# Performance work log

Measured on AMD Instinct MI355X. Metric: run time of the kernel, lower is better.

The kernel has to match this reference:

```python
import jax, jax.numpy as jnp
import numpy as np

N_NODES = 50000
N_GRAPHS = 50
MAX_NODES = 1000  # equal-size graphs
C_IN = 128
C_OUT = 128
N_EDGES = 800000
N_LAYERS = 3
BN_EPS = 1e-5


def setup_inputs() -> dict:
    key = jax.random.key(0)
    ks = jax.random.split(key, 20)
    x = jax.random.normal(ks[0], (N_NODES, C_IN), dtype=jnp.float32)
    edge_index = jax.random.randint(ks[1], (2, N_EDGES), 0, N_NODES, dtype=jnp.int64)
    batch = jnp.repeat(jnp.arange(N_GRAPHS, dtype=jnp.int64), MAX_NODES)
    s_in = 1.0 / np.sqrt(C_IN)
    s_out = 1.0 / np.sqrt(C_OUT)
    fh_W = jax.random.normal(ks[2], (C_IN, C_OUT), dtype=jnp.float32) * s_in
    fh_b = jnp.zeros((C_OUT,), dtype=jnp.float32)
    W1 = jax.random.normal(ks[3], (N_LAYERS, C_OUT, C_OUT), dtype=jnp.float32) * s_out
    b1 = jnp.zeros((N_LAYERS, C_OUT), dtype=jnp.float32)
    g1 = jnp.ones((N_LAYERS, C_OUT), dtype=jnp.float32)
    be1 = jnp.zeros((N_LAYERS, C_OUT), dtype=jnp.float32)
    W2 = jax.random.normal(ks[4], (N_LAYERS, C_OUT, C_OUT), dtype=jnp.float32) * s_out
    b2 = jnp.zeros((N_LAYERS, C_OUT), dtype=jnp.float32)
    g2 = jnp.ones((N_LAYERS, C_OUT), dtype=jnp.float32)
    be2 = jnp.zeros((N_LAYERS, C_OUT), dtype=jnp.float32)
    return {"x": x, "edge_index": edge_index, "batch": batch,
            "fh_W": fh_W, "fh_b": fh_b,
            "W1": W1, "b1": b1, "g1": g1, "be1": be1,
            "W2": W2, "b2": b2, "g2": g2, "be2": be2}


def _bn(h, gamma, beta):
    # training-mode BatchNorm1d over the node dim (biased variance, like torch)
    mu = jnp.mean(h, axis=0)
    var = jnp.var(h, axis=0)
    return (h - mu) * jax.lax.rsqrt(var + BN_EPS) * gamma + beta


def _mlp(h, W1, b1, g1, be1, W2, b2, g2, be2):
    h = jax.nn.relu(_bn(h @ W1 + b1, g1, be1))
    h = jax.nn.relu(_bn(h @ W2 + b2, g2, be2))
    return h


def _to_dense_batch(h, batch):
    # counts per graph -> exclusive starts -> intra-graph position
    ones = jnp.ones((h.shape[0],), dtype=jnp.int32)
    counts = jax.ops.segment_sum(ones, batch, num_segments=N_GRAPHS)
    starts = jnp.cumsum(counts) - counts
    pos = jnp.arange(h.shape[0], dtype=jnp.int32) - starts[batch]
    dense = jnp.zeros((N_GRAPHS, MAX_NODES, h.shape[1]), dtype=h.dtype)
    return dense.at[batch, pos].set(h)


def reference(x, edge_index, batch, fh_W, fh_b, W1, b1, g1, be1, W2, b2, g2, be2):
    src, dst = edge_index[0], edge_index[1]
    h = x @ fh_W + fh_b  # first_head Linear
    outs = [_to_dense_batch(h, batch)]
    for l in range(N_LAYERS):
        # GINConv: mlp((1+eps)*x + sum_{j->i} x_j), eps=0
        agg = jax.ops.segment_sum(h[src], dst, num_segments=N_NODES)
        h = _mlp(h + agg, W1[l], b1[l], g1[l], be1[l], W2[l], b2[l], g2[l], be2[l])
        outs.append(_to_dense_batch(h, batch))
    return jnp.stack(outs)  # [N_LAYERS+1, B, MAX_NODES, C]
```

## Files before the change

### kernel.cpp

```cpp
#include <hip/hip_runtime.h>

#define NN 50000
#define NE 800000
#define CC 128
#define SLAB (NN * CC)
#define BN_EPS 1e-5f

typedef __attribute__((ext_vector_type(8))) short bf16x8;
typedef __attribute__((ext_vector_type(4))) float f32x4;
typedef unsigned short ushort_t;

__device__ inline ushort_t f2bf(float v) {
  unsigned u = __builtin_bit_cast(unsigned, v);
  unsigned r = u + 0x7FFFu + ((u >> 16) & 1u);
  return (ushort_t)(r >> 16);
}

__global__ void zero_int_kernel(int* __restrict__ p, int n) {
  int i = blockIdx.x * blockDim.x + threadIdx.x;
  if (i < n) p[i] = 0;
}

__global__ void count_kernel(const int* __restrict__ dst, int* __restrict__ counts) {
  int e = blockIdx.x * blockDim.x + threadIdx.x;
  if (e < NE) atomicAdd(&counts[dst[e]], 1);
}

__global__ void scan1_kernel(const int* __restrict__ counts, int* __restrict__ excl,
                             int* __restrict__ blocksum) {
  __shared__ int s[256];
  int t = threadIdx.x;
  int i = blockIdx.x * 256 + t;
  int v = (i < NN) ? counts[i] : 0;
  s[t] = v;
  for (int off = 1; off < 256; off <<= 1) {
    __syncthreads();
    int add = (t >= off) ? s[t - off] : 0;
    __syncthreads();
    s[t] += add;
  }
  __syncthreads();
  if (i < NN) excl[i] = s[t] - v;
  if (t == 255) blocksum[blockIdx.x] = s[255];
}

__global__ void scan2_kernel(int* __restrict__ blocksum, int nb) {
  __shared__ int s[256];
  int t = threadIdx.x;
  int v = (t < nb) ? blocksum[t] : 0;
  s[t] = v;
  for (int off = 1; off < 256; off <<= 1) {
    __syncthreads();
    int add = (t >= off) ? s[t - off] : 0;
    __syncthreads();
    s[t] += add;
  }
  __syncthreads();
  if (t < nb) blocksum[t] = s[t] - v;
}

__global__ void scan3_kernel(int* __restrict__ excl, const int* __restrict__ blocksum) {
  int i = blockIdx.x * 256 + threadIdx.x;
  if (i < NN) excl[i] += blocksum[blockIdx.x];
}

__global__ void fill_kernel(const int* __restrict__ src, const int* __restrict__ dst,
                            const int* __restrict__ starts, int* __restrict__ fill,
                            int* __restrict__ bucket) {
  int e = blockIdx.x * blockDim.x + threadIdx.x;
  if (e < NE) {
    int d = dst[e];
    int pos = atomicAdd(&fill[d], 1);
    bucket[starts[d] + pos] = src[e];
  }
}

__global__ void prep_w_kernel(const float* __restrict__ fh_W, const float* __restrict__ W1,
                              const float* __restrict__ W2, short* __restrict__ whi,
                              short* __restrict__ wlo) {
  int m = blockIdx.x;
  const float* src = (m == 0) ? fh_W : ((m <= 3) ? W1 + (m - 1) * CC * CC : W2 + (m - 4) * CC * CC);
  short* hi = whi + m * CC * CC;
  short* lo = wlo + m * CC * CC;
  for (int it = 0; it < 64; ++it) {
    int idx = it * 256 + threadIdx.x;
    int j = idx & 7;
    int l = (idx >> 3) & 63;
    int nt = (idx >> 9) & 7;
    int ks = idx >> 12;
    int n = nt * 16 + (l & 15);
    int k = ks * 32 + ((l >> 4) << 3) + j;
    float v = src[k * CC + n];
    unsigned u = __builtin_bit_cast(unsigned, v);
    unsigned short h = (unsigned short)(u >> 16);
    float hf = __builtin_bit_cast(float, ((unsigned)h) << 16);
    float r = v - hf;
    unsigned ur = __builtin_bit_cast(unsigned, r);
    hi[idx] = (short)h;
    lo[idx] = (short)(ur >> 16);
  }
}

__global__ void gather_kernel(const ushort_t* __restrict__ h16, const int* __restrict__ starts,
                              const int* __restrict__ counts, const int* __restrict__ bucket,
                              ushort_t* __restrict__ agg16, float* __restrict__ stats) {
  if (blockIdx.x == 0) {
    stats[threadIdx.x] = 0.f;
    stats[256 + threadIdx.x] = 0.f;
  }
  const int node = blockIdx.x * 4 + (threadIdx.x >> 6);
  const int l = threadIdx.x & 63;
  const int j16 = l & 15;
  const int q = l >> 4;
  const uint4* tbl = (const uint4*)h16;

  float acc[8];
  if (q == 0) {
    uint4 u = tbl[node * 16 + j16];
    acc[0] = __builtin_bit_cast(float, u.x << 16);
    acc[1] = __builtin_bit_cast(float, u.x & 0xFFFF0000u);
    acc[2] = __builtin_bit_cast(float, u.y << 16);
    acc[3] = __builtin_bit_cast(float, u.y & 0xFFFF0000u);
    acc[4] = __builtin_bit_cast(float, u.z << 16);
    acc[5] = __builtin_bit_cast(float, u.z & 0xFFFF0000u);
    acc[6] = __builtin_bit_cast(float, u.w << 16);
    acc[7] = __builtin_bit_cast(float, u.w & 0xFFFF0000u);
  } else {
#pragma unroll
    for (int k = 0; k < 8; ++k) acc[k] = 0.f;
  }

  const int s = starts[node];
  const int n = counts[node];
  for (int base = 0; base < n; base += 64) {
    int nb = min(n - base, 64);
    int idx = (l < nb) ? bucket[s + base + l] : 0;
    int jj = 0;
    for (; jj + 8 <= nb; jj += 8) {
      int sr0 = __shfl(idx, jj + q);
      int sr1 = __shfl(idx, jj + 4 + q);
      uint4 a = tbl[sr0 * 16 + j16];
      uint4 b = tbl[sr1 * 16 + j16];
      acc[0] += __builtin_bit_cast(float, a.x << 16);
      acc[1] += __builtin_bit_cast(float, a.x & 0xFFFF0000u);
      acc[2] += __builtin_bit_cast(float, a.y << 16);
      acc[3] += __builtin_bit_cast(float, a.y & 0xFFFF0000u);
      acc[4] += __builtin_bit_cast(float, a.z << 16);
      acc[5] += __builtin_bit_cast(float, a.z & 0xFFFF0000u);
      acc[6] += __builtin_bit_cast(float, a.w << 16);
      acc[7] += __builtin_bit_cast(float, a.w & 0xFFFF0000u);
      acc[0] += __builtin_bit_cast(float, b.x << 16);
      acc[1] += __builtin_bit_cast(float, b.x & 0xFFFF0000u);
      acc[2] += __builtin_bit_cast(float, b.y << 16);
      acc[3] += __builtin_bit_cast(float, b.y & 0xFFFF0000u);
      acc[4] += __builtin_bit_cast(float, b.z << 16);
      acc[5] += __builtin_bit_cast(float, b.z & 0xFFFF0000u);
      acc[6] += __builtin_bit_cast(float, b.w << 16);
      acc[7] += __builtin_bit_cast(float, b.w & 0xFFFF0000u);
    }
    for (; jj < nb; jj += 4) {
      int i = jj + q;
      int sr = __shfl(idx, i);
      if (i < nb) {
        uint4 a = tbl[sr * 16 + j16];
        acc[0] += __builtin_bit_cast(float, a.x << 16);
        acc[1] += __builtin_bit_cast(float, a.x & 0xFFFF0000u);
        acc[2] += __builtin_bit_cast(float, a.y << 16);
        acc[3] += __builtin_bit_cast(float, a.y & 0xFFFF0000u);
        acc[4] += __builtin_bit_cast(float, a.z << 16);
        acc[5] += __builtin_bit_cast(float, a.z & 0xFFFF0000u);
        acc[6] += __builtin_bit_cast(float, a.w << 16);
        acc[7] += __builtin_bit_cast(float, a.w & 0xFFFF0000u);
      }
    }
  }
#pragma unroll
  for (int k = 0; k < 8; ++k) {
    acc[k] += __shfl_xor(acc[k], 16);
    acc[k] += __shfl_xor(acc[k], 32);
  }
  if (q == 0) {
    uint4 o;
    o.x = (unsigned)f2bf(acc[0]) | ((unsigned)f2bf(acc[1]) << 16);
    o.y = (unsigned)f2bf(acc[2]) | ((unsigned)f2bf(acc[3]) << 16);
    o.z = (unsigned)f2bf(acc[4]) | ((unsigned)f2bf(acc[5]) << 16);
    o.w = (unsigned)f2bf(acc[6]) | ((unsigned)f2bf(acc[7]) << 16);
    ((uint4*)agg16)[node * 16 + j16] = o;
  }
}

template <int MODE>
__global__ __launch_bounds__(256) void gemm_mfma_kernel(
    const void* Aop, const short* __restrict__ Wp_hi, const short* __restrict__ Wp_lo,
    const float* __restrict__ bias, float* out, ushort_t* __restrict__ h16,
    const float* __restrict__ stats_in, const float* __restrict__ g,
    const float* __restrict__ be, float* __restrict__ stats_out) {
  constexpr bool STATS = (MODE != 0);
  __shared__ float sred[2 * CC];
  const int t = threadIdx.x;
  const int l = t & 63;
  const int wv = t >> 6;
  const int m0 = blockIdx.x * 64 + wv * 16;
  const int row = m0 + (l & 15);
  const int kg = (l >> 4) * 8;
  if (STATS) sred[t] = 0.f;

  f32x4 acc[8];
#pragma unroll
  for (int i = 0; i < 8; ++i) acc[i] = (f32x4){0.f, 0.f, 0.f, 0.f};

#pragma unroll
  for (int ks = 0; ks < 4; ++ks) {
    bf16x8 ah, al;
    if (MODE == 1) {
      if (row < NN) {
        ah = *(const bf16x8*)&((const ushort_t*)Aop)[row * CC + ks * 32 + kg];
      } else {
#pragma unroll
        for (int i = 0; i < 8; ++i) ah[i] = 0;
      }
    } else {
      float av[8];
      if (row < NN) {
        const float* ap = &((const float*)Aop)[row * CC + ks * 32 + kg];
        float4 v0 = *(const float4*)ap;
        float4 v1 = *(const float4*)(ap + 4);
        av[0] = v0.x; av[1] = v0.y; av[2] = v0.z; av[3] = v0.w;
        av[4] = v1.x; av[5] = v1.y; av[6] = v1.z; av[7] = v1.w;
      } else {
#pragma unroll
        for (int i = 0; i < 8; ++i) av[i] = 0.f;
      }
      if (MODE == 2) {
#pragma unroll
        for (int i = 0; i < 8; ++i) {
          int c = ks * 32 + kg + i;
          float mu = stats_in[c] * (1.0f / NN);
          float var = stats_in[CC + c] * (1.0f / NN) - mu * mu;
          var = fmaxf(var, 0.f);
          float a = g[c] * rsqrtf(var + BN_EPS);
          float d = fmaf(-mu, a, be[c]);
          av[i] = fmaxf(fmaf(av[i], a, d), 0.f);
          ah[i] = (short)f2bf(av[i]);
        }
      } else {
#pragma unroll
        for (int i = 0; i < 8; ++i) {
          unsigned u = __builtin_bit_cast(unsigned, av[i]);
          unsigned short hbits = (unsigned short)(u >> 16);
          float hf = __builtin_bit_cast(float, ((unsigned)hbits) << 16);
          float r = av[i] - hf;
          unsigned ur = __builtin_bit_cast(unsigned, r);
          ah[i] = (short)hbits;
          al[i] = (short)(ur >> 16);
        }
      }
    }
#pragma unroll
    for (int nt = 0; nt < 8; ++nt) {
      const int base = (ks * 8 + nt) * 512 + l * 8;
      bf16x8 wh = *(const bf16x8*)&Wp_hi[base];
      bf16x8 wl = *(const bf16x8*)&Wp_lo[base];
      if (MODE == 0) {
        acc[nt] = __builtin_amdgcn_mfma_f32_16x16x32_bf16(ah, wh, acc[nt], 0, 0, 0);
        acc[nt] = __builtin_amdgcn_mfma_f32_16x16x32_bf16(al, wh, acc[nt], 0, 0, 0);
        acc[nt] = __builtin_amdgcn_mfma_f32_16x16x32_bf16(ah, wl, acc[nt], 0, 0, 0);
      } else {
        acc[nt] = __builtin_amdgcn_mfma_f32_16x16x32_bf16(ah, wh, acc[nt], 0, 0, 0);
        acc[nt] = __builtin_amdgcn_mfma_f32_16x16x32_bf16(ah, wl, acc[nt], 0, 0, 0);
      }
    }
  }

  if (STATS) __syncthreads();
  const int rbase = m0 + (l >> 4) * 4;
  const int cn = l & 15;
#pragma unroll
  for (int nt = 0; nt < 8; ++nt) {
    int c = nt * 16 + cn;
    float bv = bias[c];
    float s = 0.f, qq = 0.f;
#pragma unroll
    for (int r = 0; r < 4; ++r) {
      int rr = rbase + r;
      if (rr < NN) {
        float v = acc[nt][r] + bv;
        out[rr * CC + c] = v;
        if (MODE == 0) h16[rr * CC + c] = f2bf(v);
        if (STATS) { s += v; qq += v * v; }
      }
    }
    if (STATS) {
      s += __shfl_xor(s, 16); s += __shfl_xor(s, 32);
      qq += __shfl_xor(qq, 16); qq += __shfl_xor(qq, 32);
      if ((l >> 4) == 0) {
        atomicAdd(&sred[c], s);
        atomicAdd(&sred[CC + c], qq);
      }
    }
  }
  if (STATS) {
    __syncthreads();
    atomicAdd(&stats_out[t], sred[t]);
  }
}

__global__ void apply_kernel(const float* __restrict__ tmp, const float* __restrict__ stats2,
                             const float* __restrict__ g2, const float* __restrict__ be2,
                             float* __restrict__ outslab, ushort_t* __restrict__ h16) {
  int i = blockIdx.x * blockDim.x + threadIdx.x;
  float4 v = ((const float4*)tmp)[i];
  int c = (i & 31) << 2;
  float4 sm = *(const float4*)&stats2[c];
  float4 sq = *(const float4*)&stats2[CC + c];
  float4 gg = *(const float4*)&g2[c];
  float4 bb = *(const float4*)&be2[c];
  float4 a, d;
  {
    float mu = sm.x * (1.0f / NN), var = fmaxf(sq.x * (1.0f / NN) - mu * mu, 0.f);
    a.x = gg.x * rsqrtf(var + BN_EPS); d.x = fmaf(-mu, a.x, bb.x);
    mu = sm.y * (1.0f / NN); var = fmaxf(sq.y * (1.0f / NN) - mu * mu, 0.f);
    a.y = gg.y * rsqrtf(var + BN_EPS); d.y = fmaf(-mu, a.y, bb.y);
    mu = sm.z * (1.0f / NN); var = fmaxf(sq.z * (1.0f / NN) - mu * mu, 0.f);
    a.z = gg.z * rsqrtf(var + BN_EPS); d.z = fmaf(-mu, a.z, bb.z);
    mu = sm.w * (1.0f / NN); var = fmaxf(sq.w * (1.0f / NN) - mu * mu, 0.f);
    a.w = gg.w * rsqrtf(var + BN_EPS); d.w = fmaf(-mu, a.w, bb.w);
  }
  v.x = fmaxf(fmaf(v.x, a.x, d.x), 0.f);
  v.y = fmaxf(fmaf(v.y, a.y, d.y), 0.f);
  v.z = fmaxf(fmaf(v.z, a.z, d.z), 0.f);
  v.w = fmaxf(fmaf(v.w, a.w, d.w), 0.f);
  ((float4*)outslab)[i] = v;
  if (h16) {
    ushort_t p[4] = {f2bf(v.x), f2bf(v.y), f2bf(v.z), f2bf(v.w)};
    *(uint2*)&h16[i * 4] = *(uint2*)p;
  }
}

extern "C" void kernel_launch(void* const* d_in, const int* in_sizes, int n_in,
                              void* d_out, int out_size, void* d_ws, size_t ws_size,
                              hipStream_t stream) {
  const float* x    = (const float*)d_in[0];
  const int*   edge = (const int*)d_in[1];
  const float* fh_W = (const float*)d_in[3];
  const float* fh_b = (const float*)d_in[4];
  const float* W1   = (const float*)d_in[5];
  const float* b1   = (const float*)d_in[6];
  const float* g1   = (const float*)d_in[7];
  const float* be1  = (const float*)d_in[8];
  const float* W2   = (const float*)d_in[9];
  const float* b2   = (const float*)d_in[10];
  const float* g2   = (const float*)d_in[11];
  const float* be2  = (const float*)d_in[12];
  float* out = (float*)d_out;

  const int* src = edge;
  const int* dst = edge + NE;

  int* counts   = (int*)d_ws;
  int* fill     = counts + 50048;
  int* starts   = fill + 50048;
  int* blocksum = starts + 50048;
  int* bucket   = blocksum + 256;
  float* stats  = (float*)(bucket + NE);
  short* whi    = (short*)(stats + 512);
  short* wlo    = whi + 7 * CC * CC;
  ushort_t* h16 = (ushort_t*)(wlo + 7 * CC * CC);
  ushort_t* agg16 = h16 + SLAB;
  float* tmp    = (float*)(agg16 + SLAB);

  zero_int_kernel<<<(100096 + 255) / 256, 256, 0, stream>>>(counts, 100096);
  count_kernel<<<NE / 256, 256, 0, stream>>>(dst, counts);
  scan1_kernel<<<196, 256, 0, stream>>>(counts, starts, blocksum);
  scan2_kernel<<<1, 256, 0, stream>>>(blocksum, 196);
  scan3_kernel<<<196, 256, 0, stream>>>(starts, blocksum);
  fill_kernel<<<NE / 256, 256, 0, stream>>>(src, dst, starts, fill, bucket);

  prep_w_kernel<<<7, 256, 0, stream>>>(fh_W, W1, W2, whi, wlo);

  gemm_mfma_kernel<0><<<782, 256, 0, stream>>>(
      x, whi, wlo, fh_b, out, h16, nullptr, nullptr, nullptr, nullptr);

  for (int ly = 0; ly < 3; ++ly) {
    gather_kernel<<<NN / 4, 256, 0, stream>>>(h16, starts, counts, bucket, agg16, stats);
    gemm_mfma_kernel<1><<<782, 256, 0, stream>>>(
        agg16, whi + (1 + ly) * CC * CC, wlo + (1 + ly) * CC * CC, b1 + ly * CC,
        tmp, nullptr, nullptr, nullptr, nullptr, stats);
    gemm_mfma_kernel<2><<<782, 256, 0, stream>>>(
        tmp, whi + (4 + ly) * CC * CC, wlo + (4 + ly) * CC * CC, b2 + ly * CC,
        tmp, nullptr, stats, g1 + ly * CC, be1 + ly * CC, stats + 256);
    apply_kernel<<<SLAB / 4 / 256, 256, 0, stream>>>(
        tmp, stats + 256, g2 + ly * CC, be2 + ly * CC, out + (ly + 1) * SLAB,
        (ly < 2) ? h16 : (ushort_t*)nullptr);
  }
}
```

Baseline: 481.3 us.

## Fuse neighbor gather into first MLP GEMM and store intermediate as bf16

The neighbor-sum gather is folded into the first MLP GEMM. Each wave aggregates 16 nodes into a swizzled LDS tile and feeds it straight to MFMA, so the agg16 round trip through global memory goes away. The pre-BN intermediate between the two GEMMs is now stored as bf16 instead of fp32, which halves that traffic. BN statistics get per-layer buffers that are zeroed once up front. The cost is much less gather parallelism, since each wave walks 16 nodes one after another with fewer waves in flight, plus some precision loss from the bf16 intermediate.

```diff
diff --git a/kernel.cpp b/kernel.cpp
--- a/kernel.cpp
+++ b/kernel.cpp
@@ -14,6 +14,9 @@
   unsigned u = __builtin_bit_cast(unsigned, v);
   unsigned r = u + 0x7FFFu + ((u >> 16) & 1u);
   return (ushort_t)(r >> 16);
+}
+__device__ inline float bf2f(unsigned hi16_lo) {
+  return __builtin_bit_cast(float, hi16_lo << 16);
 }
 
 __global__ void zero_int_kernel(int* __restrict__ p, int n) {
@@ -101,101 +104,208 @@
   }
 }
 
-__global__ void gather_kernel(const ushort_t* __restrict__ h16, const int* __restrict__ starts,
-                              const int* __restrict__ counts, const int* __restrict__ bucket,
-                              ushort_t* __restrict__ agg16, float* __restrict__ stats) {
-  if (blockIdx.x == 0) {
-    stats[threadIdx.x] = 0.f;
-    stats[256 + threadIdx.x] = 0.f;
-  }
-  const int node = blockIdx.x * 4 + (threadIdx.x >> 6);
-  const int l = threadIdx.x & 63;
+__global__ __launch_bounds__(256) void gemm0_kernel(
+    const float* __restrict__ A, const short* __restrict__ Wp_hi, const short* __restrict__ Wp_lo,
+    const float* __restrict__ bias, float* __restrict__ out, ushort_t* __restrict__ h16) {
+  const int t = threadIdx.x;
+  const int l = t & 63;
+  const int wv = t >> 6;
+  const int m0 = blockIdx.x * 64 + wv * 16;
+  const int row = m0 + (l & 15);
+  const int kg = (l >> 4) * 8;
+
+  f32x4 acc[8];
+#pragma unroll
+  for (int i = 0; i < 8; ++i) acc[i] = (f32x4){0.f, 0.f, 0.f, 0.f};
+
+#pragma unroll
+  for (int ks = 0; ks < 4; ++ks) {
+    float av[8];
+    if (row < NN) {
+      const float* ap = &A[row * CC + ks * 32 + kg];
+      float4 v0 = *(const float4*)ap;
+      float4 v1 = *(const float4*)(ap + 4);
+      av[0] = v0.x; av[1] = v0.y; av[2] = v0.z; av[3] = v0.w;
+      av[4] = v1.x; av[5] = v1.y; av[6] = v1.z; av[7] = v1.w;
+    } else {
+#pragma unroll
+      for (int i = 0; i < 8; ++i) av[i] = 0.f;
+    }
+    bf16x8 ah, al;
+#pragma unroll
+    for (int i = 0; i < 8; ++i) {
+      unsigned u = __builtin_bit_cast(unsigned, av[i]);
+      unsigned short hbits = (unsigned short)(u >> 16);
+      float hf = __builtin_bit_cast(float, ((unsigned)hbits) << 16);
+      float r = av[i] - hf;
+      unsigned ur = __builtin_bit_cast(unsigned, r);
+      ah[i] = (short)hbits;
+      al[i] = (short)(ur >> 16);
+    }
+#pragma unroll
+    for (int nt = 0; nt < 8; ++nt) {
+      const int base = (ks * 8 + nt) * 512 + l * 8;
+      bf16x8 wh = *(const bf16x8*)&Wp_hi[base];
+      bf16x8 wl = *(const bf16x8*)&Wp_lo[base];
+      acc[nt] = __builtin_amdgcn_mfma_f32_16x16x32_bf16(ah, wh, acc[nt], 0, 0, 0);
+      acc[nt] = __builtin_amdgcn_mfma_f32_16x16x32_bf16(al, wh, acc[nt], 0, 0, 0);
+      acc[nt] = __builtin_amdgcn_mfma_f32_16x16x32_bf16(ah, wl, acc[nt], 0, 0, 0);
+    }
+  }
+
+  const int rbase = m0 + (l >> 4) * 4;
+  const int cn = l & 15;
+#pragma unroll
+  for (int nt = 0; nt < 8; ++nt) {
+    int c = nt * 16 + cn;
+    float bv = bias[c];
+#pragma unroll
+    for (int r = 0; r < 4; ++r) {
+      int rr = rbase + r;
+      if (rr < NN) {
+        float v = acc[nt][r] + bv;
+        out[rr * CC + c] = v;
+        h16[rr * CC + c] = f2bf(v);
+      }
+    }
+  }
+}
+
+__global__ __launch_bounds__(256) void fused1_kernel(
+    const ushort_t* __restrict__ h16, const int* __restrict__ starts,
+    const int* __restrict__ counts, const int* __restrict__ bucket,
+    const short* __restrict__ Wp_hi, const short* __restrict__ Wp_lo,
+    const float* __restrict__ bias, ushort_t* __restrict__ tmp16,
+    float* __restrict__ stats_out) {
+  __shared__ ushort_t tile[4][16][128];
+  __shared__ float sred[2 * CC];
+  const int t = threadIdx.x;
+  const int l = t & 63;
+  const int wv = t >> 6;
+  const int q = l >> 4;
   const int j16 = l & 15;
-  const int q = l >> 4;
+  const int m0 = blockIdx.x * 64 + wv * 16;
+  sred[t] = 0.f;
+
   const uint4* tbl = (const uint4*)h16;
 
-  float acc[8];
-  if (q == 0) {
-    uint4 u = tbl[node * 16 + j16];
-    acc[0] = __builtin_bit_cast(float, u.x << 16);
-    acc[1] = __builtin_bit_cast(float, u.x & 0xFFFF0000u);
-    acc[2] = __builtin_bit_cast(float, u.y << 16);
-    acc[3] = __builtin_bit_cast(float, u.y & 0xFFFF0000u);
-    acc[4] = __builtin_bit_cast(float, u.z << 16);
-    acc[5] = __builtin_bit_cast(float, u.z & 0xFFFF0000u);
-    acc[6] = __builtin_bit_cast(float, u.w << 16);
-    acc[7] = __builtin_bit_cast(float, u.w & 0xFFFF0000u);
-  } else {
+  for (int j = 0; j < 16; ++j) {
+    const int node = m0 + j;
+    float acc[8];
 #pragma unroll
     for (int k = 0; k < 8; ++k) acc[k] = 0.f;
-  }
-
-  const int s = starts[node];
-  const int n = counts[node];
-  for (int base = 0; base < n; base += 64) {
-    int nb = min(n - base, 64);
-    int idx = (l < nb) ? bucket[s + base + l] : 0;
-    int jj = 0;
-    for (; jj + 8 <= nb; jj += 8) {
-      int sr0 = __shfl(idx, jj + q);
-      int sr1 = __shfl(idx, jj + 4 + q);
-      uint4 a = tbl[sr0 * 16 + j16];
-      uint4 b = tbl[sr1 * 16 + j16];
-      acc[0] += __builtin_bit_cast(float, a.x << 16);
-      acc[1] += __builtin_bit_cast(float, a.x & 0xFFFF0000u);
-      acc[2] += __builtin_bit_cast(float, a.y << 16);
-      acc[3] += __builtin_bit_cast(float, a.y & 0xFFFF0000u);
-      acc[4] += __builtin_bit_cast(float, a.z << 16);
-      acc[5] += __builtin_bit_cast(float, a.z & 0xFFFF0000u);
-      acc[6] += __builtin_bit_cast(float, a.w << 16);
-      acc[7] += __builtin_bit_cast(float, a.w & 0xFFFF0000u);
-      acc[0] += __builtin_bit_cast(float, b.x << 16);
-      acc[1] += __builtin_bit_cast(float, b.x & 0xFFFF0000u);
-      acc[2] += __builtin_bit_cast(float, b.y << 16);
-      acc[3] += __builtin_bit_cast(float, b.y & 0xFFFF0000u);
-      acc[4] += __builtin_bit_cast(float, b.z << 16);
-      acc[5] += __builtin_bit_cast(float, b.z & 0xFFFF0000u);
-      acc[6] += __builtin_bit_cast(float, b.w << 16);
-      acc[7] += __builtin_bit_cast(float, b.w & 0xFFFF0000u);
-    }
-    for (; jj < nb; jj += 4) {
-      int i = jj + q;
-      int sr = __shfl(idx, i);
-      if (i < nb) {
-        uint4 a = tbl[sr * 16 + j16];
-        acc[0] += __builtin_bit_cast(float, a.x << 16);
-        acc[1] += __builtin_bit_cast(float, a.x & 0xFFFF0000u);
-        acc[2] += __builtin_bit_cast(float, a.y << 16);
-        acc[3] += __builtin_bit_cast(float, a.y & 0xFFFF0000u);
-        acc[4] += __builtin_bit_cast(float, a.z << 16);
-        acc[5] += __builtin_bit_cast(float, a.z & 0xFFFF0000u);
-        acc[6] += __builtin_bit_cast(float, a.w << 16);
-        acc[7] += __builtin_bit_cast(float, a.w & 0xFFFF0000u);
-      }
-    }
-  }
-#pragma unroll
-  for (int k = 0; k < 8; ++k) {
-    acc[k] += __shfl_xor(acc[k], 16);
-    acc[k] += __shfl_xor(acc[k], 32);
-  }
-  if (q == 0) {
-    uint4 o;
-    o.x = (unsigned)f2bf(acc[0]) | ((unsigned)f2bf(acc[1]) << 16);
-    o.y = (unsigned)f2bf(acc[2]) | ((unsigned)f2bf(acc[3]) << 16);
-    o.z = (unsigned)f2bf(acc[4]) | ((unsigned)f2bf(acc[5]) << 16);
-    o.w = (unsigned)f2bf(acc[6]) | ((unsigned)f2bf(acc[7]) << 16);
-    ((uint4*)agg16)[node * 16 + j16] = o;
-  }
-}
-
-template <int MODE>
-__global__ __launch_bounds__(256) void gemm_mfma_kernel(
-    const void* Aop, const short* __restrict__ Wp_hi, const short* __restrict__ Wp_lo,
-    const float* __restrict__ bias, float* out, ushort_t* __restrict__ h16,
+    if (node < NN) {
+      if (q == 0) {
+        uint4 u = tbl[node * 16 + j16];
+        acc[0] = bf2f(u.x & 0xFFFF); acc[1] = bf2f(u.x >> 16);
+        acc[2] = bf2f(u.y & 0xFFFF); acc[3] = bf2f(u.y >> 16);
+        acc[4] = bf2f(u.z & 0xFFFF); acc[5] = bf2f(u.z >> 16);
+        acc[6] = bf2f(u.w & 0xFFFF); acc[7] = bf2f(u.w >> 16);
+      }
+      const int s = starts[node];
+      const int n = counts[node];
+      for (int base = 0; base < n; base += 64) {
+        int nb = min(n - base, 64);
+        int idx = (l < nb) ? bucket[s + base + l] : 0;
+        int jj = 0;
+        for (; jj + 16 <= nb; jj += 16) {
+          int sr0 = __shfl(idx, jj + q);
+          int sr1 = __shfl(idx, jj + 4 + q);
+          int sr2 = __shfl(idx, jj + 8 + q);
+          int sr3 = __shfl(idx, jj + 12 + q);
+          uint4 a = tbl[sr0 * 16 + j16];
+          uint4 b = tbl[sr1 * 16 + j16];
+          uint4 cc2 = tbl[sr2 * 16 + j16];
+          uint4 d = tbl[sr3 * 16 + j16];
+          acc[0] += bf2f(a.x & 0xFFFF) + bf2f(b.x & 0xFFFF) + bf2f(cc2.x & 0xFFFF) + bf2f(d.x & 0xFFFF);
+          acc[1] += bf2f(a.x >> 16) + bf2f(b.x >> 16) + bf2f(cc2.x >> 16) + bf2f(d.x >> 16);
+          acc[2] += bf2f(a.y & 0xFFFF) + bf2f(b.y & 0xFFFF) + bf2f(cc2.y & 0xFFFF) + bf2f(d.y & 0xFFFF);
+          acc[3] += bf2f(a.y >> 16) + bf2f(b.y >> 16) + bf2f(cc2.y >> 16) + bf2f(d.y >> 16);
+          acc[4] += bf2f(a.z & 0xFFFF) + bf2f(b.z & 0xFFFF) + bf2f(cc2.z & 0xFFFF) + bf2f(d.z & 0xFFFF);
+          acc[5] += bf2f(a.z >> 16) + bf2f(b.z >> 16) + bf2f(cc2.z >> 16) + bf2f(d.z >> 16);
+          acc[6] += bf2f(a.w & 0xFFFF) + bf2f(b.w & 0xFFFF) + bf2f(cc2.w & 0xFFFF) + bf2f(d.w & 0xFFFF);
+          acc[7] += bf2f(a.w >> 16) + bf2f(b.w >> 16) + bf2f(cc2.w >> 16) + bf2f(d.w >> 16);
+        }
+        for (; jj < nb; jj += 4) {
+          int i = jj + q;
+          int sr = __shfl(idx, (i < nb) ? i : (nb - 1));
+          if (i < nb) {
+            uint4 a = tbl[sr * 16 + j16];
+            acc[0] += bf2f(a.x & 0xFFFF); acc[1] += bf2f(a.x >> 16);
+            acc[2] += bf2f(a.y & 0xFFFF); acc[3] += bf2f(a.y >> 16);
+            acc[4] += bf2f(a.z & 0xFFFF); acc[5] += bf2f(a.z >> 16);
+            acc[6] += bf2f(a.w & 0xFFFF); acc[7] += bf2f(a.w >> 16);
+          }
+        }
+      }
+#pragma unroll
+      for (int k = 0; k < 8; ++k) {
+        acc[k] += __shfl_xor(acc[k], 16);
+        acc[k] += __shfl_xor(acc[k], 32);
+      }
+    }
+    if (q == 0) {
+      uint4 o;
+      o.x = (unsigned)f2bf(acc[0]) | ((unsigned)f2bf(acc[1]) << 16);
+      o.y = (unsigned)f2bf(acc[2]) | ((unsigned)f2bf(acc[3]) << 16);
+      o.z = (unsigned)f2bf(acc[4]) | ((unsigned)f2bf(acc[5]) << 16);
+      o.w = (unsigned)f2bf(acc[6]) | ((unsigned)f2bf(acc[7]) << 16);
+      int byteoff = (j16 * 16) ^ ((j & 7) << 4);
+      *(uint4*)((char*)&tile[wv][j][0] + byteoff) = o;
+    }
+  }
+  __syncthreads();
+
+  f32x4 acc2[8];
+#pragma unroll
+  for (int i = 0; i < 8; ++i) acc2[i] = (f32x4){0.f, 0.f, 0.f, 0.f};
+
+#pragma unroll
+  for (int ks = 0; ks < 4; ++ks) {
+    int byteoff = ((ks * 4 + q) * 16) ^ ((j16 & 7) << 4);
+    bf16x8 ah = *(const bf16x8*)((const char*)&tile[wv][j16][0] + byteoff);
+#pragma unroll
+    for (int nt = 0; nt < 8; ++nt) {
+      const int base = (ks * 8 + nt) * 512 + l * 8;
+      bf16x8 wh = *(const bf16x8*)&Wp_hi[base];
+      bf16x8 wl = *(const bf16x8*)&Wp_lo[base];
+      acc2[nt] = __builtin_amdgcn_mfma_f32_16x16x32_bf16(ah, wh, acc2[nt], 0, 0, 0);
+      acc2[nt] = __builtin_amdgcn_mfma_f32_16x16x32_bf16(ah, wl, acc2[nt], 0, 0, 0);
+    }
+  }
+
+  const int rbase = m0 + (l >> 4) * 4;
+  const int cn = l & 15;
+#pragma unroll
+  for (int nt = 0; nt < 8; ++nt) {
+    int c = nt * 16 + cn;
+    float bv = bias[c];
+    float s = 0.f, qq = 0.f;
+#pragma unroll
+    for (int r = 0; r < 4; ++r) {
+      int rr = rbase + r;
+      if (rr < NN) {
+        float v = acc2[nt][r] + bv;
+        tmp16[rr * CC + c] = f2bf(v);
+        s += v; qq += v * v;
+      }
+    }
+    s += __shfl_xor(s, 16); s += __shfl_xor(s, 32);
+    qq += __shfl_xor(qq, 16); qq += __shfl_xor(qq, 32);
+    if (q == 0) {
+      atomicAdd(&sred[c], s);
+      atomicAdd(&sred[CC + c], qq);
+    }
+  }
+  __syncthreads();
+  atomicAdd(&stats_out[t], sred[t]);
+}
+
+__global__ __launch_bounds__(256) void gemm2_kernel(
+    const ushort_t* __restrict__ tmp16, const short* __restrict__ Wp_hi,
+    const short* __restrict__ Wp_lo, const float* __restrict__ bias,
     const float* __restrict__ stats_in, const float* __restrict__ g,
-    const float* __restrict__ be, float* __restrict__ stats_out) {
-  constexpr bool STATS = (MODE != 0);
+    const float* __restrict__ be, float* __restrict__ tmp2, float* __restrict__ stats_out) {
   __shared__ float sred[2 * CC];
   const int t = threadIdx.x;
   const int l = t & 63;
@@ -203,7 +313,7 @@
   const int m0 = blockIdx.x * 64 + wv * 16;
   const int row = m0 + (l & 15);
   const int kg = (l >> 4) * 8;
-  if (STATS) sred[t] = 0.f;
+  sred[t] = 0.f;
 
   f32x4 acc[8];
 #pragma unroll
@@ -211,68 +321,35 @@
 
 #pragma unroll
   for (int ks = 0; ks < 4; ++ks) {
-    bf16x8 ah, al;
-    if (MODE == 1) {
-      if (row < NN) {
-        ah = *(const bf16x8*)&((const ushort_t*)Aop)[row * CC + ks * 32 + kg];
-      } else {
-#pragma unroll
-        for (int i = 0; i < 8; ++i) ah[i] = 0;
+    bf16x8 ah;
+    if (row < NN) {
+      bf16x8 raw = *(const bf16x8*)&tmp16[row * CC + ks * 32 + kg];
+#pragma unroll
+      for (int i = 0; i < 8; ++i) {
+        int c = ks * 32 + kg + i;
+        float mu = stats_in[c] * (1.0f / NN);
+        float var = fmaxf(stats_in[CC + c] * (1.0f / NN) - mu * mu, 0.f);
+        float a = g[c] * rsqrtf(var + BN_EPS);
+        float d = fmaf(-mu, a, be[c]);
+        float v = bf2f((unsigned)(ushort_t)raw[i]);
+        v = fmaxf(fmaf(v, a, d), 0.f);
+        ah[i] = (short)f2bf(v);
       }
     } else {
-      float av[8];
-      if (row < NN) {
-        const float* ap = &((const float*)Aop)[row * CC + ks * 32 + kg];
-        float4 v0 = *(const float4*)ap;
-        float4 v1 = *(const float4*)(ap + 4);
-        av[0] = v0.x; av[1] = v0.y; av[2] = v0.z; av[3] = v0.w;
-        av[4] = v1.x; av[5] = v1.y; av[6] = v1.z; av[7] = v1.w;
-      } else {
-#pragma unroll
-        for (int i = 0; i < 8; ++i) av[i] = 0.f;
-      }
-      if (MODE == 2) {
-#pragma unroll
-        for (int i = 0; i < 8; ++i) {
-          int c = ks * 32 + kg + i;
-          float mu = stats_in[c] * (1.0f / NN);
-          float var = stats_in[CC + c] * (1.0f / NN) - mu * mu;
-          var = fmaxf(var, 0.f);
-          float a = g[c] * rsqrtf(var + BN_EPS);
-          float d = fmaf(-mu, a, be[c]);
-          av[i] = fmaxf(fmaf(av[i], a, d), 0.f);
-          ah[i] = (short)f2bf(av[i]);
-        }
-      } else {
-#pragma unroll
-        for (int i = 0; i < 8; ++i) {
-          unsigned u = __builtin_bit_cast(unsigned, av[i]);
-          unsigned short hbits = (unsigned short)(u >> 16);
-          float hf = __builtin_bit_cast(float, ((unsigned)hbits) << 16);
-          float r = av[i] - hf;
-          unsigned ur = __builtin_bit_cast(unsigned, r);
-          ah[i] = (short)hbits;
-          al[i] = (short)(ur >> 16);
-        }
-      }
+#pragma unroll
+      for (int i = 0; i < 8; ++i) ah[i] = 0;
     }
 #pragma unroll
     for (int nt = 0; nt < 8; ++nt) {
       const int base = (ks * 8 + nt) * 512 + l * 8;
       bf16x8 wh = *(const bf16x8*)&Wp_hi[base];
       bf16x8 wl = *(const bf16x8*)&Wp_lo[base];
-      if (MODE == 0) {
-        acc[nt] = __builtin_amdgcn_mfma_f32_16x16x32_bf16(ah, wh, acc[nt], 0, 0, 0);
-        acc[nt] = __builtin_amdgcn_mfma_f32_16x16x32_bf16(al, wh, acc[nt], 0, 0, 0);
-        acc[nt] = __builtin_amdgcn_mfma_f32_16x16x32_bf16(ah, wl, acc[nt], 0, 0, 0);
-      } else {
-        acc[nt] = __builtin_amdgcn_mfma_f32_16x16x32_bf16(ah, wh, acc[nt], 0, 0, 0);
-        acc[nt] = __builtin_amdgcn_mfma_f32_16x16x32_bf16(ah, wl, acc[nt], 0, 0, 0);
-      }
-    }
-  }
-
-  if (STATS) __syncthreads();
+      acc[nt] = __builtin_amdgcn_mfma_f32_16x16x32_bf16(ah, wh, acc[nt], 0, 0, 0);
+      acc[nt] = __builtin_amdgcn_mfma_f32_16x16x32_bf16(ah, wl, acc[nt], 0, 0, 0);
+    }
+  }
+
+  __syncthreads();
   const int rbase = m0 + (l >> 4) * 4;
   const int cn = l & 15;
 #pragma unroll
@@ -285,24 +362,19 @@
       int rr = rbase + r;
       if (rr < NN) {
         float v = acc[nt][r] + bv;
-        out[rr * CC + c] = v;
-        if (MODE == 0) h16[rr * CC + c] = f2bf(v);
-        if (STATS) { s += v; qq += v * v; }
-      }
-    }
-    if (STATS) {
-      s += __shfl_xor(s, 16); s += __shfl_xor(s, 32);
-      qq += __shfl_xor(qq, 16); qq += __shfl_xor(qq, 32);
-      if ((l >> 4) == 0) {
-        atomicAdd(&sred[c], s);
-        atomicAdd(&sred[CC + c], qq);
-      }
-    }
-  }
-  if (STATS) {
-    __syncthreads();
-    atomicAdd(&stats_out[t], sred[t]);
-  }
+        tmp2[rr * CC + c] = v;
+        s += v; qq += v * v;
+      }
+    }
+    s += __shfl_xor(s, 16); s += __shfl_xor(s, 32);
+    qq += __shfl_xor(qq, 16); qq += __shfl_xor(qq, 32);
+    if ((l >> 4) == 0) {
+      atomicAdd(&sred[c], s);
+      atomicAdd(&sred[CC + c], qq);
+    }
+  }
+  __syncthreads();
+  atomicAdd(&stats_out[t], sred[t]);
 }
 
 __global__ void apply_kernel(const float* __restrict__ tmp, const float* __restrict__ stats2,
@@ -359,17 +431,17 @@
 
   int* counts   = (int*)d_ws;
   int* fill     = counts + 50048;
-  int* starts   = fill + 50048;
+  float* stats  = (float*)(fill + 50048);
+  int* starts   = (int*)(stats + 1536);
   int* blocksum = starts + 50048;
   int* bucket   = blocksum + 256;
-  float* stats  = (float*)(bucket + NE);
-  short* whi    = (short*)(stats + 512);
+  short* whi    = (short*)(bucket + NE);
   short* wlo    = whi + 7 * CC * CC;
   ushort_t* h16 = (ushort_t*)(wlo + 7 * CC * CC);
-  ushort_t* agg16 = h16 + SLAB;
-  float* tmp    = (float*)(agg16 + SLAB);
-
-  zero_int_kernel<<<(100096 + 255) / 256, 256, 0, stream>>>(counts, 100096);
+  ushort_t* tmp16 = h16 + SLAB;
+  float* tmp2   = (float*)(tmp16 + SLAB);
+
+  zero_int_kernel<<<(101632 + 255) / 256, 256, 0, stream>>>(counts, 101632);
   count_kernel<<<NE / 256, 256, 0, stream>>>(dst, counts);
   scan1_kernel<<<196, 256, 0, stream>>>(counts, starts, blocksum);
   scan2_kernel<<<1, 256, 0, stream>>>(blocksum, 196);
@@ -378,19 +450,19 @@
 
   prep_w_kernel<<<7, 256, 0, stream>>>(fh_W, W1, W2, whi, wlo);
 
-  gemm_mfma_kernel<0><<<782, 256, 0, stream>>>(
-      x, whi, wlo, fh_b, out, h16, nullptr, nullptr, nullptr, nullptr);
+  gemm0_kernel<<<782, 256, 0, stream>>>(x, whi, wlo, fh_b, out, h16);
 
   for (int ly = 0; ly < 3; ++ly) {
-    gather_kernel<<<NN / 4, 256, 0, stream>>>(h16, starts, counts, bucket, agg16, stats);
-    gemm_mfma_kernel<1><<<782, 256, 0, stream>>>(
-        agg16, whi + (1 + ly) * CC * CC, wlo + (1 + ly) * CC * CC, b1 + ly * CC,
-        tmp, nullptr, nullptr, nullptr, nullptr, stats);
-    gemm_mfma_kernel<2><<<782, 256, 0, stream>>>(
-        tmp, whi + (4 + ly) * CC * CC, wlo + (4 + ly) * CC * CC, b2 + ly * CC,
-        tmp, nullptr, stats, g1 + ly * CC, be1 + ly * CC, stats + 256);
+    float* stats1 = stats + (ly * 2) * 256;
+    float* stats2 = stats + (ly * 2 + 1) * 256;
+    fused1_kernel<<<782, 256, 0, stream>>>(
+        h16, starts, counts, bucket, whi + (1 + ly) * CC * CC, wlo + (1 + ly) * CC * CC,
+        b1 + ly * CC, tmp16, stats1);
+    gemm2_kernel<<<782, 256, 0, stream>>>(
+        tmp16, whi + (4 + ly) * CC * CC, wlo + (4 + ly) * CC * CC, b2 + ly * CC,
+        stats1, g1 + ly * CC, be1 + ly * CC, tmp2, stats2);
     apply_kernel<<<SLAB / 4 / 256, 256, 0, stream>>>(
-        tmp, stats + 256, g2 + ly * CC, be2 + ly * CC, out + (ly + 1) * SLAB,
+        tmp2, stats2, g2 + ly * CC, be2 + ly * CC, out + (ly + 1) * SLAB,
         (ly < 2) ? h16 : (ushort_t*)nullptr);
   }
 }
```

Result: slower. 497.8 us (+3.4%).
